# Kernel tuning notes

Measured on AMD Instinct MI355X. Metric: run time of the kernel, lower is better.

## Reference

```python
import jax, jax.numpy as jnp
import numpy as np

B, D, C, T = 2, 1024, 256, 32
H = 8
F = C // H
E = 1024  # time_embed_dim
GROUPS = 32
SCALE = F ** -0.5


def group_norm(x, scale, bias):
    # x: [B, D, C, T]; GroupNorm(32, C) over (channels-in-group, T)
    b, d, c, t = x.shape
    xg = x.reshape(b, d, GROUPS, c // GROUPS, t)
    m = xg.mean(axis=(3, 4), keepdims=True)
    v = xg.var(axis=(3, 4), keepdims=True)
    xn = ((xg - m) * jax.lax.rsqrt(v + 1e-5)).reshape(b, d, c, t)
    return xn * scale[None, None, :, None] + bias[None, None, :, None]


def rpe_R(temb, pairwise, dw, db, tw, tb, ow, ob):
    # pairwise: [B, T, T] int -> R: [B, T, T, H, F]
    pd = pairwise.astype(jnp.float32)
    dist_embs = jnp.stack([
        jnp.log1p(jnp.maximum(pd, 0.0)),
        jnp.log1p(jnp.maximum(-pd, 0.0)),
        (pairwise == 0).astype(jnp.float32),
    ], axis=-1)  # [B, T, T, 3]
    emb = (temb @ tw.T + tb)[:, :, None, :] + (dist_embs @ dw.T + db)  # [B,T,T,C]
    r = jax.nn.silu(emb) @ ow.T + ob
    return r.reshape(r.shape[0], r.shape[1], r.shape[2], H, F)


def setup_inputs() -> dict:
    key = jax.random.key(0)
    ks = jax.random.split(key, 20)
    s = 0.02
    inp = {
        "x": jax.random.normal(ks[0], (B, D, C, T), jnp.float32),
        "temb": jax.random.normal(ks[1], (B, T, E), jnp.float32),
        "norm_scale": jnp.ones((C,), jnp.float32),
        "norm_bias": jnp.zeros((C,), jnp.float32),
        "qkv_w": jax.random.normal(ks[2], (3 * C, C), jnp.float32) * s,
        "qkv_b": jnp.zeros((3 * C,), jnp.float32),
        "proj_w": jax.random.normal(ks[3], (C, C), jnp.float32) * s,
        "proj_b": jnp.zeros((C,), jnp.float32),
        # stacked RPE params for (q, k, v) nets
        "rpe_dist_w": jax.random.normal(ks[4], (3, C, 3), jnp.float32) * s,
        "rpe_dist_b": jnp.zeros((3, C), jnp.float32),
        "rpe_time_w": jax.random.normal(ks[5], (3, C, E), jnp.float32) * s,
        "rpe_time_b": jnp.zeros((3, C), jnp.float32),
        "rpe_out_w": jax.random.normal(ks[6], (3, C, C), jnp.float32) * s,
        "rpe_out_b": jax.random.normal(ks[7], (3, C), jnp.float32) * s,
        "frame_indices": jnp.sort(jax.random.randint(ks[8], (B, T), 0, 100), axis=-1),
    }
    return inp


def reference(x, temb, norm_scale, norm_bias, qkv_w, qkv_b, proj_w, proj_b,
              rpe_dist_w, rpe_dist_b, rpe_time_w, rpe_time_b, rpe_out_w, rpe_out_b,
              frame_indices):
    xn = group_norm(x, norm_scale, norm_bias)          # [B,D,C,T]
    xt = jnp.einsum('BDCT->BDTC', xn)                  # [B,D,T,C]
    qkv = (xt @ qkv_w.T + qkv_b).reshape(B, D, T, 3, H, F)
    qkv = jnp.einsum('BDTtHF->tBDHTF', qkv)
    q, k, v = qkv[0] * SCALE, qkv[1], qkv[2]           # [B,D,H,T,F]

    attn = jnp.einsum('bdhtf,bdhsf->bdhts', q, k)

    pairwise = frame_indices[:, :, None] - frame_indices[:, None, :]  # [B,T,T]
    R_q = rpe_R(temb, pairwise, rpe_dist_w[0], rpe_dist_b[0], rpe_time_w[0], rpe_time_b[0], rpe_out_w[0], rpe_out_b[0])
    R_k = rpe_R(temb, pairwise, rpe_dist_w[1], rpe_dist_b[1], rpe_time_w[1], rpe_time_b[1], rpe_out_w[1], rpe_out_b[1])
    R_v = rpe_R(temb, pairwise, rpe_dist_w[2], rpe_dist_b[2], rpe_time_w[2], rpe_time_b[2], rpe_out_w[2], rpe_out_b[2])

    attn = attn + jnp.einsum('bdhtf,btshf->bdhts', q, R_k)
    # rpe_q: forward_qk on (k*scale) then transpose last two dims
    attn = attn + jnp.einsum('bdhtf,btshf->bdhts', k * SCALE, R_q).swapaxes(-1, -2)

    attn = jax.nn.softmax(attn.astype(jnp.float32), axis=-1).astype(attn.dtype)

    out = jnp.einsum('bdhts,bdhsf->bdhtf', attn, v)
    out = out + jnp.einsum('bdhts,btshf->bdhtf', attn, R_v)

    out = jnp.einsum('BDHTF->BDTHF', out).reshape(B, D, T, C)
    out = out @ proj_w.T + proj_b
    y = xt + out                                       # residual on post-norm x (as in source)
    return jnp.einsum('BDTC->BDCT', y)
```

## Files before the change

### kernel.cpp

```cpp
#include <hip/hip_runtime.h>

#define BB 2
#define DD 1024
#define CC 256
#define TT 32
#define HH 8
#define FF 32
#define EE 1024
#define SCALE 0.17677669529663687f

typedef unsigned short u16;
typedef unsigned int u32;
typedef __attribute__((ext_vector_type(8))) short s8v;
typedef __attribute__((ext_vector_type(4))) float f32x4;

static __device__ __forceinline__ float u2f(u16 u) {
  return __uint_as_float(((u32)u) << 16);
}
static __device__ __forceinline__ u16 f2u(float f) {
  u32 x = __float_as_uint(f);
  x += 0x7fffu + ((x >> 16) & 1u);
  return (u16)(x >> 16);
}
static __device__ __forceinline__ float dot2bf(u32 a, u32 b, float c) {
  float d;
  asm("v_dot2_f32_bf16 %0, %1, %2, %3" : "=v"(d) : "v"(a), "v"(b), "v"(c));
  return d;
}
#define D2(acc, a, b) acc = dot2bf(a, b, acc)

static __device__ __forceinline__ float logits_r(
    const u16* kr,
    uint4 r0, uint4 r1, uint4 r2, uint4 r3,
    uint4 r4, uint4 r5, uint4 r6, uint4 r7,
    uint4 q0, uint4 q1, uint4 q2, uint4 q3) {
  uint4 k0 = *(const uint4*)(kr + 0);
  uint4 k1 = *(const uint4*)(kr + 8);
  uint4 k2 = *(const uint4*)(kr + 16);
  uint4 k3 = *(const uint4*)(kr + 24);
  float xq = 0.f, xr = 0.f, xk = 0.f;
  D2(xq, q0.x, k0.x); D2(xq, q0.y, k0.y); D2(xq, q0.z, k0.z); D2(xq, q0.w, k0.w);
  D2(xq, q1.x, k1.x); D2(xq, q1.y, k1.y); D2(xq, q1.z, k1.z); D2(xq, q1.w, k1.w);
  D2(xq, q2.x, k2.x); D2(xq, q2.y, k2.y); D2(xq, q2.z, k2.z); D2(xq, q2.w, k2.w);
  D2(xq, q3.x, k3.x); D2(xq, q3.y, k3.y); D2(xq, q3.z, k3.z); D2(xq, q3.w, k3.w);
  D2(xr, q0.x, r0.x); D2(xr, q0.y, r0.y); D2(xr, q0.z, r0.z); D2(xr, q0.w, r0.w);
  D2(xr, q1.x, r1.x); D2(xr, q1.y, r1.y); D2(xr, q1.z, r1.z); D2(xr, q1.w, r1.w);
  D2(xr, q2.x, r2.x); D2(xr, q2.y, r2.y); D2(xr, q2.z, r2.z); D2(xr, q2.w, r2.w);
  D2(xr, q3.x, r3.x); D2(xr, q3.y, r3.y); D2(xr, q3.z, r3.z); D2(xr, q3.w, r3.w);
  D2(xk, k0.x, r4.x); D2(xk, k0.y, r4.y); D2(xk, k0.z, r4.z); D2(xk, k0.w, r4.w);
  D2(xk, k1.x, r5.x); D2(xk, k1.y, r5.y); D2(xk, k1.z, r5.z); D2(xk, k1.w, r5.w);
  D2(xk, k2.x, r6.x); D2(xk, k2.y, r6.y); D2(xk, k2.z, r6.z); D2(xk, k2.w, r6.w);
  D2(xk, k3.x, r7.x); D2(xk, k3.y, r7.y); D2(xk, k3.z, r7.z); D2(xk, k3.w, r7.w);
  return xq + xr + xk;
}

static __device__ __forceinline__ float pv_r(
    uint4 p0, uint4 p1, uint4 p2, uint4 p3,
    const u16* vr, uint4 r0, uint4 r1, uint4 r2, uint4 r3) {
  uint4 v0 = *(const uint4*)(vr + 0),  v1 = *(const uint4*)(vr + 8);
  uint4 v2 = *(const uint4*)(vr + 16), v3 = *(const uint4*)(vr + 24);
  float o = 0.f;
  D2(o, p0.x, v0.x); D2(o, p0.y, v0.y); D2(o, p0.z, v0.z); D2(o, p0.w, v0.w);
  D2(o, p1.x, v1.x); D2(o, p1.y, v1.y); D2(o, p1.z, v1.z); D2(o, p1.w, v1.w);
  D2(o, p2.x, v2.x); D2(o, p2.y, v2.y); D2(o, p2.z, v2.z); D2(o, p2.w, v2.w);
  D2(o, p3.x, v3.x); D2(o, p3.y, v3.y); D2(o, p3.z, v3.z); D2(o, p3.w, v3.w);
  D2(o, p0.x, r0.x); D2(o, p0.y, r0.y); D2(o, p0.z, r0.z); D2(o, p0.w, r0.w);
  D2(o, p1.x, r1.x); D2(o, p1.y, r1.y); D2(o, p1.z, r1.z); D2(o, p1.w, r1.w);
  D2(o, p2.x, r2.x); D2(o, p2.y, r2.y); D2(o, p2.z, r2.z); D2(o, p2.w, r2.w);
  D2(o, p3.x, r3.x); D2(o, p3.y, r3.y); D2(o, p3.z, r3.z); D2(o, p3.w, r3.w);
  return o;
}

#define LOADROW8(P, v0, v1, v2, v3, v4, v5, v6, v7)                      \
  v0 = *(const uint4*)((P) + 0);  v1 = *(const uint4*)((P) + 8);         \
  v2 = *(const uint4*)((P) + 16); v3 = *(const uint4*)((P) + 24);        \
  v4 = *(const uint4*)((P) + 32); v5 = *(const uint4*)((P) + 40);        \
  v6 = *(const uint4*)((P) + 48); v7 = *(const uint4*)((P) + 56);
#define LOADROW4(P, v0, v1, v2, v3)                                      \
  v0 = *(const uint4*)((P) + 0);  v1 = *(const uint4*)((P) + 8);         \
  v2 = *(const uint4*)((P) + 16); v3 = *(const uint4*)((P) + 24);

__global__ void k_prep(const float* __restrict__ qw, const float* __restrict__ pw,
                       const float* __restrict__ ow, const float* __restrict__ tw,
                       u16* __restrict__ wpk2, u16* __restrict__ ppk,
                       u16* __restrict__ opk, float* __restrict__ twT) {
  int id = blockIdx.x * 256 + threadIdx.x;
  if (id < 24576) {
    int lane = id & 63, ks = (id >> 6) & 7, tile = id >> 9;
    int hh = tile / 6, r = tile % 6, sec = r >> 1, nt = r & 1;
    int nrow = sec * 256 + hh * 32 + nt * 16 + (lane & 15);
    int k = ks * 32 + (lane >> 4) * 8;
    const float* src = qw + (size_t)nrow * 256 + k;
    u16* dst = wpk2 + (size_t)id * 8;
#pragma unroll
    for (int e = 0; e < 8; ++e) dst[e] = f2u(src[e]);
  } else if (id < 32768) {
    int j = id - 24576;
    int lane = j & 63, ks = (j >> 6) & 7, nt = j >> 9;
    int row = nt * 16 + (lane & 15);
    int k = ks * 32 + (lane >> 4) * 8;
    const float* src = pw + (size_t)row * 256 + k;
    u16* dst = ppk + (size_t)j * 8;
#pragma unroll
    for (int e = 0; e < 8; ++e) dst[e] = f2u(src[e]);
  } else if (id < 57344) {
    int j = id - 32768;
    int lane = j & 63, ks = (j >> 6) & 7, g = j >> 9;
    int n = g >> 4, ntg = g & 15;
    int row = ntg * 16 + (lane & 15);
    int k = ks * 32 + (lane >> 4) * 8;
    const float* src = ow + ((size_t)n * 256 + row) * 256 + k;
    u16* dst = opk + (size_t)j * 8;
#pragma unroll
    for (int e = 0; e < 8; ++e) dst[e] = f2u(src[e]);
  } else {
    int j = id - 57344;
    int n = j >> 16, r = j & 65535;
    int e = r >> 6, c0 = (r & 63) * 4;
    float4 v;
    v.x = tw[((size_t)n * 256 + c0 + 0) * 1024 + e];
    v.y = tw[((size_t)n * 256 + c0 + 1) * 1024 + e];
    v.z = tw[((size_t)n * 256 + c0 + 2) * 1024 + e];
    v.w = tw[((size_t)n * 256 + c0 + 3) * 1024 + e];
    *(float4*)(twT + (size_t)n * 262144 + (size_t)e * 256 + c0) = v;
  }
}

__global__ __launch_bounds__(256) void k_tpe(
    const float* __restrict__ temb, const float* __restrict__ twT,
    const float* __restrict__ tb, const float* __restrict__ dw,
    const float* __restrict__ db, const int* __restrict__ fidx,
    u16* __restrict__ E) {
  int bid = blockIdx.x;
  int t = bid & 31, b = (bid >> 5) & 1, n = bid >> 6;
  __shared__ float st[EE];
  __shared__ int sfi[TT];
  for (int e = threadIdx.x; e < EE; e += 256)
    st[e] = temb[((size_t)b * TT + t) * EE + e];
  if (threadIdx.x < TT) sfi[threadIdx.x] = fidx[b * TT + threadIdx.x];
  __syncthreads();
  int c = threadIdx.x;
  const float* wp = twT + (size_t)n * 262144 + c;
  float a0 = 0.f, a1 = 0.f, a2 = 0.f, a3 = 0.f;
  for (int e = 0; e < EE; e += 4) {
    a0 += st[e + 0] * wp[(size_t)(e + 0) * 256];
    a1 += st[e + 1] * wp[(size_t)(e + 1) * 256];
    a2 += st[e + 2] * wp[(size_t)(e + 2) * 256];
    a3 += st[e + 3] * wp[(size_t)(e + 3) * 256];
  }
  float base = a0 + a1 + a2 + a3 + tb[n * 256 + c] + db[n * 256 + c];
  float dw0 = dw[(n * 256 + c) * 3 + 0];
  float dw1 = dw[(n * 256 + c) * 3 + 1];
  float dw2 = dw[(n * 256 + c) * 3 + 2];
  int ft = sfi[t];
  u16* erow = E + ((size_t)n * 2048 + b * 1024 + t * 32) * 256 + c;
  for (int s = 0; s < TT; ++s) {
    int pd = ft - sfi[s];
    float d0 = log1pf((float)(pd > 0 ? pd : 0));
    float d1 = log1pf((float)(pd < 0 ? -pd : 0));
    float d2 = (pd == 0) ? 1.f : 0.f;
    float e = base + d0 * dw0 + d1 * dw1 + d2 * dw2;
    float se = e / (1.f + expf(-e));
    erow[(size_t)s * 256] = f2u(se);
  }
}

__global__ __launch_bounds__(256) void k_rgemm(
    const u16* __restrict__ E, const u16* __restrict__ opk,
    const float* __restrict__ ob,
    u16* __restrict__ RKQ, u16* __restrict__ Rv) {
  int bid = blockIdx.x;
  int n = bid >> 6, rem = bid & 63;
  int mblk = rem >> 1, nblk = rem & 1;
  int tid = threadIdx.x;
  int w = tid >> 6, lane = tid & 63;
  int l15 = lane & 15, l4 = lane >> 4;
  size_t rowbase = (size_t)n * 2048 + mblk * 64;

  f32x4 acc[2][4];
#pragma unroll
  for (int i = 0; i < 2; ++i) {
    int ntg = nblk * 8 + w * 2 + i;
    float ov = ob[n * 256 + ntg * 16 + l15];
#pragma unroll
    for (int mt = 0; mt < 4; ++mt) acc[i][mt] = (f32x4){ov, ov, ov, ov};
  }
  for (int ks = 0; ks < 8; ++ks) {
    s8v a[4];
#pragma unroll
    for (int mt = 0; mt < 4; ++mt)
      a[mt] = *(const s8v*)(E + (rowbase + mt * 16 + l15) * 256 + ks * 32 + l4 * 8);
#pragma unroll
    for (int i = 0; i < 2; ++i) {
      int ntg = nblk * 8 + w * 2 + i;
      s8v bf = *(const s8v*)(opk + (((size_t)(n * 16 + ntg) * 8 + ks) * 64 + lane) * 8);
#pragma unroll
      for (int mt = 0; mt < 4; ++mt)
        acc[i][mt] = __builtin_amdgcn_mfma_f32_16x16x32_bf16(a[mt], bf, acc[i][mt], 0, 0, 0);
    }
  }
#pragma unroll
  for (int i = 0; i < 2; ++i) {
    int cc = (nblk * 8 + w * 2 + i) * 16 + l15;
    int hh = cc >> 5, f = cc & 31;
#pragma unroll
    for (int mt = 0; mt < 4; ++mt)
#pragma unroll
      for (int r = 0; r < 4; ++r) {
        int rloc = mblk * 64 + mt * 16 + l4 * 4 + r;
        int bb2 = rloc >> 10, tt = (rloc >> 5) & 31, ss = rloc & 31;
        size_t bh = (size_t)(bb2 * 8 + hh);
        float v = acc[i][mt][r];
        if (n == 0)      RKQ[(bh * 1024 + ss * 32 + tt) * 64 + 32 + f] = f2u(v * SCALE);
        else if (n == 1) RKQ[(bh * 1024 + tt * 32 + ss) * 64 + f] = f2u(v);
        else             Rv[((bh * 32 + tt) * 32 + f) * 32 + ss] = f2u(v);
      }
  }
}

__global__ __launch_bounds__(256, 4) void k_gn(
    const float* __restrict__ x, const float* __restrict__ nsc,
    const float* __restrict__ nbi, u16* __restrict__ pun) {
  int bid = blockIdx.x;
  int xcd = bid & 7, jj = bid >> 3;
  int b = xcd >> 2;
  int d = (xcd & 3) * 256 + jj;
  const int tid = threadIdx.x;
  __shared__ u16 xt[TT][264];
  const size_t xbase = ((size_t)(b * DD + d)) * 8192;
  u16* xnp = pun + xbase * 2 + 8192;
  {
    const int c0 = tid >> 3, tq = tid & 7;
    for (int c = c0; c < CC; c += 32) {
      float4 v = *(const float4*)(x + xbase + (size_t)c * TT + tq * 4);
      xt[tq * 4 + 0][c] = f2u(v.x);
      xt[tq * 4 + 1][c] = f2u(v.y);
      xt[tq * 4 + 2][c] = f2u(v.z);
      xt[tq * 4 + 3][c] = f2u(v.w);
    }
  }
  __syncthreads();
  {
    const int c = tid;
    float s = 0.f, s2 = 0.f;
    for (int t = 0; t < TT; ++t) { float v = u2f(xt[t][c]); s += v; s2 += v * v; }
    s += __shfl_xor(s, 1); s2 += __shfl_xor(s2, 1);
    s += __shfl_xor(s, 2); s2 += __shfl_xor(s2, 2);
    s += __shfl_xor(s, 4); s2 += __shfl_xor(s2, 4);
    const float mean = s * (1.f / 256.f);
    const float var = s2 * (1.f / 256.f) - mean * mean;
    const float rs = rsqrtf(var + 1e-5f);
    const float scv = nsc[c] * rs;
    const float biv = nbi[c] - mean * scv;
    for (int t = 0; t < TT; ++t) xt[t][c] = f2u(u2f(xt[t][c]) * scv + biv);
  }
  __syncthreads();
#pragma unroll
  for (int it = 0; it < 4; ++it) {
    int u = it * 256 + tid;
    int t = u >> 5, c = (u & 31) * 8;
    *(uint4*)(xnp + (size_t)u * 8) = *(const uint4*)&xt[t][c];
  }
}

__global__ __launch_bounds__(256, 3) void k_attn(
    u16* __restrict__ pun, const u16* __restrict__ wpk2,
    const float* __restrict__ qkb,
    const u16* __restrict__ RKQ, const u16* __restrict__ Rv) {
  int bid = blockIdx.x;
  int xcd = bid & 7, i5 = bid >> 3;
  int b = xcd >> 2;
  int h = i5 & 7;
  int dg = (xcd & 3) * 64 + (i5 >> 3);
  int d0 = dg * 4;
  const int tid = threadIdx.x;
  __shared__ u16 xsbuf[32 * 264];
  __shared__ u16 qs[4][32][40];
  __shared__ u16 ks_[4][32][40];
  __shared__ u16 vT[4][32][40];
#define XS_(r, c)   xsbuf[(r) * 264 + (c)]
#define ATSP(d, t)  (xsbuf + ((d) * 32 + (t)) * 40)

  const int w = tid >> 6, lane = tid & 63;
  const int l15 = lane & 15, l4 = lane >> 4;
  const int t = tid >> 3, j = tid & 7;
  const size_t bh = (size_t)(b * 8 + h);
  const u16* rp0 = RKQ + (bh * 1024 + (size_t)t * 32 + j) * 64;
  const u16* rv0 = Rv + ((bh * 32 + (size_t)t) * 32 + j) * 32;

  u16* slot0 = pun + ((size_t)(b * DD + d0)) * 16384;

  const u16* xp0 = slot0 + 8192;
  uint4 xr0 = *(const uint4*)(xp0 + (size_t)tid * 8);
  uint4 xr1 = *(const uint4*)(xp0 + (size_t)(256 + tid) * 8);
  uint4 xr2 = *(const uint4*)(xp0 + (size_t)(512 + tid) * 8);
  uint4 xr3 = *(const uint4*)(xp0 + (size_t)(768 + tid) * 8);

  for (int d = 0; d < 4; ++d) {
    *(uint4*)&XS_((tid >> 5), (tid & 31) * 8) = xr0;
    *(uint4*)&XS_(8 + (tid >> 5), (tid & 31) * 8) = xr1;
    *(uint4*)&XS_(16 + (tid >> 5), (tid & 31) * 8) = xr2;
    *(uint4*)&XS_(24 + (tid >> 5), (tid & 31) * 8) = xr3;
    __syncthreads();
    if (d < 3) {
      const u16* nx = slot0 + (size_t)(d + 1) * 16384 + 8192;
      xr0 = *(const uint4*)(nx + (size_t)tid * 8);
      xr1 = *(const uint4*)(nx + (size_t)(256 + tid) * 8);
      xr2 = *(const uint4*)(nx + (size_t)(512 + tid) * 8);
      xr3 = *(const uint4*)(nx + (size_t)(768 + tid) * 8);
    }
#pragma unroll
    for (int i = 0; i < 3; ++i) {
      const int u = w * 3 + i;
      const int sec = u >> 2;
      const int nt = (u >> 1) & 1;
      const int mh = u & 1;
      f32x4 acc = {0.f, 0.f, 0.f, 0.f};
      const u16* wb = wpk2 + ((size_t)((h * 6 + sec * 2 + nt) * 8) * 64 + lane) * 8;
      for (int ks = 0; ks < 8; ++ks) {
        s8v a = *(const s8v*)&XS_(mh * 16 + l15, ks * 32 + l4 * 8);
        s8v bf = *(const s8v*)(wb + (size_t)ks * 512);
        acc = __builtin_amdgcn_mfma_f32_16x16x32_bf16(a, bf, acc, 0, 0, 0);
      }
      const int f = nt * 16 + l15;
      const float bias = qkb[sec * 256 + h * 32 + f];
#pragma unroll
      for (int r = 0; r < 4; ++r) {
        const int tt = mh * 16 + l4 * 4 + r;
        const float val = acc[r] + bias;
        if (sec == 0)      qs[d][tt][f] = f2u(val * SCALE);
        else if (sec == 1) ks_[d][tt][f] = f2u(val);
        else               vT[d][f][tt] = f2u(val);
      }
    }
    __syncthreads();
  }

  uint4 q[4][4];
#pragma unroll
  for (int d = 0; d < 4; ++d) {
    q[d][0] = *(const uint4*)&qs[d][t][0];
    q[d][1] = *(const uint4*)&qs[d][t][8];
    q[d][2] = *(const uint4*)&qs[d][t][16];
    q[d][3] = *(const uint4*)&qs[d][t][24];
  }
  float a[4][4];
  uint4 A0, A1, A2, A3, A4, A5, A6, A7;
  uint4 B0, B1, B2, B3, B4, B5, B6, B7;
  LOADROW8(rp0,          A0, A1, A2, A3, A4, A5, A6, A7)
  LOADROW8(rp0 + 8 * 64, B0, B1, B2, B3, B4, B5, B6, B7)
#pragma unroll
  for (int d = 0; d < 4; ++d)
    a[d][0] = logits_r(&ks_[d][j][0], A0, A1, A2, A3, A4, A5, A6, A7,
                       q[d][0], q[d][1], q[d][2], q[d][3]);
  LOADROW8(rp0 + 16 * 64, A0, A1, A2, A3, A4, A5, A6, A7)
#pragma unroll
  for (int d = 0; d < 4; ++d)
    a[d][1] = logits_r(&ks_[d][j + 8][0], B0, B1, B2, B3, B4, B5, B6, B7,
                       q[d][0], q[d][1], q[d][2], q[d][3]);
  LOADROW8(rp0 + 24 * 64, B0, B1, B2, B3, B4, B5, B6, B7)
#pragma unroll
  for (int d = 0; d < 4; ++d)
    a[d][2] = logits_r(&ks_[d][j + 16][0], A0, A1, A2, A3, A4, A5, A6, A7,
                       q[d][0], q[d][1], q[d][2], q[d][3]);
#pragma unroll
  for (int d = 0; d < 4; ++d)
    a[d][3] = logits_r(&ks_[d][j + 24][0], B0, B1, B2, B3, B4, B5, B6, B7,
                       q[d][0], q[d][1], q[d][2], q[d][3]);

#pragma unroll
  for (int d = 0; d < 4; ++d) {
    float mx = fmaxf(fmaxf(a[d][0], a[d][1]), fmaxf(a[d][2], a[d][3]));
    mx = fmaxf(mx, __shfl_xor(mx, 1));
    mx = fmaxf(mx, __shfl_xor(mx, 2));
    mx = fmaxf(mx, __shfl_xor(mx, 4));
    float e0 = __expf(a[d][0] - mx), e1 = __expf(a[d][1] - mx);
    float e2 = __expf(a[d][2] - mx), e3 = __expf(a[d][3] - mx);
    float sum = e0 + e1 + e2 + e3;
    sum += __shfl_xor(sum, 1);
    sum += __shfl_xor(sum, 2);
    sum += __shfl_xor(sum, 4);
    const float inv = 1.f / sum;
    u16* ap = ATSP(d, t);
    ap[j]      = f2u(e0 * inv);
    ap[j + 8]  = f2u(e1 * inv);
    ap[j + 16] = f2u(e2 * inv);
    ap[j + 24] = f2u(e3 * inv);
  }

  uint4 p[4][4];
#pragma unroll
  for (int d = 0; d < 4; ++d) {
    const u16* ap = ATSP(d, t);
    p[d][0] = *(const uint4*)(ap + 0);
    p[d][1] = *(const uint4*)(ap + 8);
    p[d][2] = *(const uint4*)(ap + 16);
    p[d][3] = *(const uint4*)(ap + 24);
  }
  float o[4][4];
  uint4 VA0, VA1, VA2, VA3, VB0, VB1, VB2, VB3;
  LOADROW4(rv0,          VA0, VA1, VA2, VA3)
  LOADROW4(rv0 + 8 * 32, VB0, VB1, VB2, VB3)
#pragma unroll
  for (int d = 0; d < 4; ++d)
    o[d][0] = pv_r(p[d][0], p[d][1], p[d][2], p[d][3], &vT[d][j][0],
                   VA0, VA1, VA2, VA3);
  LOADROW4(rv0 + 16 * 32, VA0, VA1, VA2, VA3)
#pragma unroll
  for (int d = 0; d < 4; ++d)
    o[d][1] = pv_r(p[d][0], p[d][1], p[d][2], p[d][3], &vT[d][j + 8][0],
                   VB0, VB1, VB2, VB3);
  LOADROW4(rv0 + 24 * 32, VB0, VB1, VB2, VB3)
#pragma unroll
  for (int d = 0; d < 4; ++d)
    o[d][2] = pv_r(p[d][0], p[d][1], p[d][2], p[d][3], &vT[d][j + 16][0],
                   VA0, VA1, VA2, VA3);
#pragma unroll
  for (int d = 0; d < 4; ++d)
    o[d][3] = pv_r(p[d][0], p[d][1], p[d][2], p[d][3], &vT[d][j + 24][0],
                   VB0, VB1, VB2, VB3);

#pragma unroll
  for (int d = 0; d < 4; ++d) {
    u16* op = slot0 + (size_t)d * 16384 + (size_t)t * 256 + h * 32 + j;
    op[0]  = f2u(o[d][0]);
    op[8]  = f2u(o[d][1]);
    op[16] = f2u(o[d][2]);
    op[24] = f2u(o[d][3]);
  }
#undef XS_
#undef ATSP
}

__global__ __launch_bounds__(256, 4) void k_proj(
    u16* __restrict__ pun, const u16* __restrict__ ppk,
    const float* __restrict__ pb, float* __restrict__ out) {
  int bid = blockIdx.x;
  int xcd = bid & 7, jj = bid >> 3;
  int b = xcd >> 2;
  int d = (xcd & 3) * 256 + jj;
  const int tid = threadIdx.x;
  __shared__ u16 obuf[32][264];
  __shared__ u16 xs[32][264];
  const size_t nbase = ((size_t)(b * DD + d)) * 8192;
  u16* slot = pun + nbase * 2;
#pragma unroll
  for (int it = 0; it < 4; ++it) {
    int u = it * 256 + tid;
    int t = u >> 5, c = (u & 31) * 8;
    *(uint4*)&obuf[t][c] = *(const uint4*)(slot + (size_t)u * 8);
    *(uint4*)&xs[t][c]   = *(const uint4*)(slot + 8192 + (size_t)u * 8);
  }
  __syncthreads();

  const int w = tid >> 6, lane = tid & 63;
  const int l15 = lane & 15, l4 = lane >> 4;
  f32x4 pacc[4][2];
#pragma unroll
  for (int i = 0; i < 4; ++i) {
    pacc[i][0] = (f32x4){0.f, 0.f, 0.f, 0.f};
    pacc[i][1] = (f32x4){0.f, 0.f, 0.f, 0.f};
  }
  for (int ks = 0; ks < 8; ++ks) {
    s8v a0 = *(const s8v*)&obuf[l15][ks * 32 + l4 * 8];
    s8v a1 = *(const s8v*)&obuf[16 + l15][ks * 32 + l4 * 8];
#pragma unroll
    for (int i = 0; i < 4; ++i) {
      s8v bf = *(const s8v*)(ppk + ((size_t)((w * 4 + i) * 8 + ks) * 64 + lane) * 8);
      pacc[i][0] = __builtin_amdgcn_mfma_f32_16x16x32_bf16(a0, bf, pacc[i][0], 0, 0, 0);
      pacc[i][1] = __builtin_amdgcn_mfma_f32_16x16x32_bf16(a1, bf, pacc[i][1], 0, 0, 0);
    }
  }
#pragma unroll
  for (int i = 0; i < 4; ++i) {
    const int co = (w * 4 + i) * 16 + l15;
    const float pbv = pb[co];
#pragma unroll
    for (int mt = 0; mt < 2; ++mt) {
      const int t0 = mt * 16 + l4 * 4;
      float4 sv;
      sv.x = pacc[i][mt][0] + u2f(xs[t0 + 0][co]) + pbv;
      sv.y = pacc[i][mt][1] + u2f(xs[t0 + 1][co]) + pbv;
      sv.z = pacc[i][mt][2] + u2f(xs[t0 + 2][co]) + pbv;
      sv.w = pacc[i][mt][3] + u2f(xs[t0 + 3][co]) + pbv;
      *(float4*)(out + nbase + (size_t)co * TT + t0) = sv;
    }
  }
}

extern "C" void kernel_launch(void* const* d_in, const int* in_sizes, int n_in,
                              void* d_out, int out_size, void* d_ws, size_t ws_size,
                              hipStream_t stream) {
  const float* x      = (const float*)d_in[0];
  const float* temb   = (const float*)d_in[1];
  const float* nsc    = (const float*)d_in[2];
  const float* nbi    = (const float*)d_in[3];
  const float* qkv_w  = (const float*)d_in[4];
  const float* qkv_b  = (const float*)d_in[5];
  const float* proj_w = (const float*)d_in[6];
  const float* proj_b = (const float*)d_in[7];
  const float* dw     = (const float*)d_in[8];
  const float* db     = (const float*)d_in[9];
  const float* tw     = (const float*)d_in[10];
  const float* tb     = (const float*)d_in[11];
  const float* ow     = (const float*)d_in[12];
  const float* ob     = (const float*)d_in[13];
  const int*   fidx   = (const int*)d_in[14];
  float* out = (float*)d_out;
  u16* pun = (u16*)d_out;

  float* twT = (float*)d_ws;
  u16* wpk2 = (u16*)(twT + 786432);
  u16* ppk  = wpk2 + 196608;
  u16* opk  = ppk + 65536;
  u16* E    = opk + 196608;
  u16* RKQ  = E + 1572864;
  u16* Rv   = RKQ + 1048576;

  k_prep<<<992, 256, 0, stream>>>(qkv_w, proj_w, ow, tw, wpk2, ppk, opk, twT);
  k_tpe<<<192, 256, 0, stream>>>(temb, twT, tb, dw, db, fidx, E);
  k_rgemm<<<192, 256, 0, stream>>>(E, opk, ob, RKQ, Rv);
  k_gn<<<2048, 256, 0, stream>>>(x, nsc, nbi, pun);
  k_attn<<<4096, 256, 0, stream>>>(pun, wpk2, qkv_b, RKQ, Rv);
  k_proj<<<2048, 256, 0, stream>>>(pun, ppk, proj_b, out);
}
```

Measured before the change: 249.0 us.

## Merge groupnorm, weight packing and time-embedding into one launch; hoist QKV weights

Combines the groupnorm, weight-packing and time-embedding projection kernels into a single heterogeneous launch, chosen by block index, so the independent stages run concurrently and two launches are saved. The time-embedding projection now reads the original row-major weights with coalesced float4 loads and a warp-shuffle reduction, which removes the separate transpose pass and the twT workspace. In the attention kernel the packed QKV weight fragments are loaded into registers once rather than once per d iteration. This raises register pressure in k_attn and may lower occupancy, and the fused kernel carries the larger combined shared-memory footprint in every block.

```diff
diff --git a/kernel.cpp b/kernel.cpp
--- a/kernel.cpp
+++ b/kernel.cpp
@@ -80,88 +80,132 @@
   v0 = *(const uint4*)((P) + 0);  v1 = *(const uint4*)((P) + 8);         \
   v2 = *(const uint4*)((P) + 16); v3 = *(const uint4*)((P) + 24);
 
-__global__ void k_prep(const float* __restrict__ qw, const float* __restrict__ pw,
-                       const float* __restrict__ ow, const float* __restrict__ tw,
-                       u16* __restrict__ wpk2, u16* __restrict__ ppk,
-                       u16* __restrict__ opk, float* __restrict__ twT) {
-  int id = blockIdx.x * 256 + threadIdx.x;
-  if (id < 24576) {
-    int lane = id & 63, ks = (id >> 6) & 7, tile = id >> 9;
-    int hh = tile / 6, r = tile % 6, sec = r >> 1, nt = r & 1;
-    int nrow = sec * 256 + hh * 32 + nt * 16 + (lane & 15);
-    int k = ks * 32 + (lane >> 4) * 8;
-    const float* src = qw + (size_t)nrow * 256 + k;
-    u16* dst = wpk2 + (size_t)id * 8;
-#pragma unroll
-    for (int e = 0; e < 8; ++e) dst[e] = f2u(src[e]);
-  } else if (id < 32768) {
-    int j = id - 24576;
-    int lane = j & 63, ks = (j >> 6) & 7, nt = j >> 9;
-    int row = nt * 16 + (lane & 15);
-    int k = ks * 32 + (lane >> 4) * 8;
-    const float* src = pw + (size_t)row * 256 + k;
-    u16* dst = ppk + (size_t)j * 8;
-#pragma unroll
-    for (int e = 0; e < 8; ++e) dst[e] = f2u(src[e]);
-  } else if (id < 57344) {
-    int j = id - 32768;
-    int lane = j & 63, ks = (j >> 6) & 7, g = j >> 9;
-    int n = g >> 4, ntg = g & 15;
-    int row = ntg * 16 + (lane & 15);
-    int k = ks * 32 + (lane >> 4) * 8;
-    const float* src = ow + ((size_t)n * 256 + row) * 256 + k;
-    u16* dst = opk + (size_t)j * 8;
-#pragma unroll
-    for (int e = 0; e < 8; ++e) dst[e] = f2u(src[e]);
+__global__ __launch_bounds__(256, 4) void k_f0(
+    const float* __restrict__ x, const float* __restrict__ nsc,
+    const float* __restrict__ nbi, u16* __restrict__ pun,
+    const float* __restrict__ qw, const float* __restrict__ pw,
+    const float* __restrict__ ow, const float* __restrict__ tw,
+    const float* __restrict__ temb, const float* __restrict__ tb,
+    const float* __restrict__ dw, const float* __restrict__ db,
+    const int* __restrict__ fidx,
+    u16* __restrict__ wpk2, u16* __restrict__ ppk, u16* __restrict__ opk,
+    u16* __restrict__ E) {
+  const int bid = blockIdx.x;
+  const int tid = threadIdx.x;
+  __shared__ u16 xt[TT][264];
+  __shared__ float st[EE];
+  __shared__ float base_s[CC];
+  __shared__ int sfi[TT];
+
+  if (bid < 2048) {
+    int xcd = bid & 7, jj = bid >> 3;
+    int b = xcd >> 2;
+    int d = (xcd & 3) * 256 + jj;
+    const size_t xbase = ((size_t)(b * DD + d)) * 8192;
+    u16* xnp = pun + xbase * 2 + 8192;
+    {
+      const int c0 = tid >> 3, tq = tid & 7;
+      for (int c = c0; c < CC; c += 32) {
+        float4 v = *(const float4*)(x + xbase + (size_t)c * TT + tq * 4);
+        xt[tq * 4 + 0][c] = f2u(v.x);
+        xt[tq * 4 + 1][c] = f2u(v.y);
+        xt[tq * 4 + 2][c] = f2u(v.z);
+        xt[tq * 4 + 3][c] = f2u(v.w);
+      }
+    }
+    __syncthreads();
+    {
+      const int c = tid;
+      float s = 0.f, s2 = 0.f;
+      for (int t = 0; t < TT; ++t) { float v = u2f(xt[t][c]); s += v; s2 += v * v; }
+      s += __shfl_xor(s, 1); s2 += __shfl_xor(s2, 1);
+      s += __shfl_xor(s, 2); s2 += __shfl_xor(s2, 2);
+      s += __shfl_xor(s, 4); s2 += __shfl_xor(s2, 4);
+      const float mean = s * (1.f / 256.f);
+      const float var = s2 * (1.f / 256.f) - mean * mean;
+      const float rs = rsqrtf(var + 1e-5f);
+      const float scv = nsc[c] * rs;
+      const float biv = nbi[c] - mean * scv;
+      for (int t = 0; t < TT; ++t) xt[t][c] = f2u(u2f(xt[t][c]) * scv + biv);
+    }
+    __syncthreads();
+#pragma unroll
+    for (int it = 0; it < 4; ++it) {
+      int u = it * 256 + tid;
+      int t = u >> 5, c = (u & 31) * 8;
+      *(uint4*)(xnp + (size_t)u * 8) = *(const uint4*)&xt[t][c];
+    }
+  } else if (bid < 2272) {
+    int id = (bid - 2048) * 256 + tid;
+    if (id < 24576) {
+      int lane = id & 63, ks = (id >> 6) & 7, tile = id >> 9;
+      int hh = tile / 6, r = tile % 6, sec = r >> 1, nt = r & 1;
+      int nrow = sec * 256 + hh * 32 + nt * 16 + (lane & 15);
+      int k = ks * 32 + (lane >> 4) * 8;
+      const float* src = qw + (size_t)nrow * 256 + k;
+      u16* dst = wpk2 + (size_t)id * 8;
+#pragma unroll
+      for (int e = 0; e < 8; ++e) dst[e] = f2u(src[e]);
+    } else if (id < 32768) {
+      int j = id - 24576;
+      int lane = j & 63, ks = (j >> 6) & 7, nt = j >> 9;
+      int row = nt * 16 + (lane & 15);
+      int k = ks * 32 + (lane >> 4) * 8;
+      const float* src = pw + (size_t)row * 256 + k;
+      u16* dst = ppk + (size_t)j * 8;
+#pragma unroll
+      for (int e = 0; e < 8; ++e) dst[e] = f2u(src[e]);
+    } else {
+      int j = id - 32768;
+      int lane = j & 63, ks = (j >> 6) & 7, g = j >> 9;
+      int n = g >> 4, ntg = g & 15;
+      int row = ntg * 16 + (lane & 15);
+      int k = ks * 32 + (lane >> 4) * 8;
+      const float* src = ow + ((size_t)n * 256 + row) * 256 + k;
+      u16* dst = opk + (size_t)j * 8;
+#pragma unroll
+      for (int e = 0; e < 8; ++e) dst[e] = f2u(src[e]);
+    }
   } else {
-    int j = id - 57344;
-    int n = j >> 16, r = j & 65535;
-    int e = r >> 6, c0 = (r & 63) * 4;
-    float4 v;
-    v.x = tw[((size_t)n * 256 + c0 + 0) * 1024 + e];
-    v.y = tw[((size_t)n * 256 + c0 + 1) * 1024 + e];
-    v.z = tw[((size_t)n * 256 + c0 + 2) * 1024 + e];
-    v.w = tw[((size_t)n * 256 + c0 + 3) * 1024 + e];
-    *(float4*)(twT + (size_t)n * 262144 + (size_t)e * 256 + c0) = v;
-  }
-}
-
-__global__ __launch_bounds__(256) void k_tpe(
-    const float* __restrict__ temb, const float* __restrict__ twT,
-    const float* __restrict__ tb, const float* __restrict__ dw,
-    const float* __restrict__ db, const int* __restrict__ fidx,
-    u16* __restrict__ E) {
-  int bid = blockIdx.x;
-  int t = bid & 31, b = (bid >> 5) & 1, n = bid >> 6;
-  __shared__ float st[EE];
-  __shared__ int sfi[TT];
-  for (int e = threadIdx.x; e < EE; e += 256)
-    st[e] = temb[((size_t)b * TT + t) * EE + e];
-  if (threadIdx.x < TT) sfi[threadIdx.x] = fidx[b * TT + threadIdx.x];
-  __syncthreads();
-  int c = threadIdx.x;
-  const float* wp = twT + (size_t)n * 262144 + c;
-  float a0 = 0.f, a1 = 0.f, a2 = 0.f, a3 = 0.f;
-  for (int e = 0; e < EE; e += 4) {
-    a0 += st[e + 0] * wp[(size_t)(e + 0) * 256];
-    a1 += st[e + 1] * wp[(size_t)(e + 1) * 256];
-    a2 += st[e + 2] * wp[(size_t)(e + 2) * 256];
-    a3 += st[e + 3] * wp[(size_t)(e + 3) * 256];
-  }
-  float base = a0 + a1 + a2 + a3 + tb[n * 256 + c] + db[n * 256 + c];
-  float dw0 = dw[(n * 256 + c) * 3 + 0];
-  float dw1 = dw[(n * 256 + c) * 3 + 1];
-  float dw2 = dw[(n * 256 + c) * 3 + 2];
-  int ft = sfi[t];
-  u16* erow = E + ((size_t)n * 2048 + b * 1024 + t * 32) * 256 + c;
-  for (int s = 0; s < TT; ++s) {
-    int pd = ft - sfi[s];
-    float d0 = log1pf((float)(pd > 0 ? pd : 0));
-    float d1 = log1pf((float)(pd < 0 ? -pd : 0));
-    float d2 = (pd == 0) ? 1.f : 0.f;
-    float e = base + d0 * dw0 + d1 * dw1 + d2 * dw2;
-    float se = e / (1.f + expf(-e));
-    erow[(size_t)s * 256] = f2u(se);
+    int bid3 = bid - 2272;
+    int t = bid3 & 31, b = (bid3 >> 5) & 1, n = bid3 >> 6;
+    for (int e = tid; e < EE; e += 256)
+      st[e] = temb[((size_t)b * TT + t) * EE + e];
+    if (tid < TT) sfi[tid] = fidx[b * TT + tid];
+    __syncthreads();
+    const int g = tid & 7, cl = tid >> 3;
+#pragma unroll
+    for (int pass = 0; pass < 8; ++pass) {
+      const int c = pass * 32 + cl;
+      const float* wr = tw + ((size_t)n * 256 + c) * 1024 + g * 4;
+      float acc = 0.f;
+      for (int step = 0; step < 32; ++step) {
+        float4 wv = *(const float4*)(wr + step * 32);
+        float4 sv = *(const float4*)(st + g * 4 + step * 32);
+        acc += sv.x * wv.x + sv.y * wv.y + sv.z * wv.z + sv.w * wv.w;
+      }
+      acc += __shfl_xor(acc, 1);
+      acc += __shfl_xor(acc, 2);
+      acc += __shfl_xor(acc, 4);
+      if (g == 0) base_s[c] = acc;
+    }
+    __syncthreads();
+    const int c = tid;
+    float base = base_s[c] + tb[n * 256 + c] + db[n * 256 + c];
+    float dw0 = dw[(n * 256 + c) * 3 + 0];
+    float dw1 = dw[(n * 256 + c) * 3 + 1];
+    float dw2 = dw[(n * 256 + c) * 3 + 2];
+    int ft = sfi[t];
+    u16* erow = E + ((size_t)n * 2048 + b * 1024 + t * 32) * 256 + c;
+    for (int s = 0; s < TT; ++s) {
+      int pd = ft - sfi[s];
+      float d0 = log1pf((float)(pd > 0 ? pd : 0));
+      float d1 = log1pf((float)(pd < 0 ? -pd : 0));
+      float d2 = (pd == 0) ? 1.f : 0.f;
+      float e = base + d0 * dw0 + d1 * dw1 + d2 * dw2;
+      float se = e / (1.f + expf(-e));
+      erow[(size_t)s * 256] = f2u(se);
+    }
   }
 }
 
@@ -215,51 +259,6 @@
         else if (n == 1) RKQ[(bh * 1024 + tt * 32 + ss) * 64 + f] = f2u(v);
         else             Rv[((bh * 32 + tt) * 32 + f) * 32 + ss] = f2u(v);
       }
-  }
-}
-
-__global__ __launch_bounds__(256, 4) void k_gn(
-    const float* __restrict__ x, const float* __restrict__ nsc,
-    const float* __restrict__ nbi, u16* __restrict__ pun) {
-  int bid = blockIdx.x;
-  int xcd = bid & 7, jj = bid >> 3;
-  int b = xcd >> 2;
-  int d = (xcd & 3) * 256 + jj;
-  const int tid = threadIdx.x;
-  __shared__ u16 xt[TT][264];
-  const size_t xbase = ((size_t)(b * DD + d)) * 8192;
-  u16* xnp = pun + xbase * 2 + 8192;
-  {
-    const int c0 = tid >> 3, tq = tid & 7;
-    for (int c = c0; c < CC; c += 32) {
-      float4 v = *(const float4*)(x + xbase + (size_t)c * TT + tq * 4);
-      xt[tq * 4 + 0][c] = f2u(v.x);
-      xt[tq * 4 + 1][c] = f2u(v.y);
-      xt[tq * 4 + 2][c] = f2u(v.z);
-      xt[tq * 4 + 3][c] = f2u(v.w);
-    }
-  }
-  __syncthreads();
-  {
-    const int c = tid;
-    float s = 0.f, s2 = 0.f;
-    for (int t = 0; t < TT; ++t) { float v = u2f(xt[t][c]); s += v; s2 += v * v; }
-    s += __shfl_xor(s, 1); s2 += __shfl_xor(s2, 1);
-    s += __shfl_xor(s, 2); s2 += __shfl_xor(s2, 2);
-    s += __shfl_xor(s, 4); s2 += __shfl_xor(s2, 4);
-    const float mean = s * (1.f / 256.f);
-    const float var = s2 * (1.f / 256.f) - mean * mean;
-    const float rs = rsqrtf(var + 1e-5f);
-    const float scv = nsc[c] * rs;
-    const float biv = nbi[c] - mean * scv;
-    for (int t = 0; t < TT; ++t) xt[t][c] = f2u(u2f(xt[t][c]) * scv + biv);
-  }
-  __syncthreads();
-#pragma unroll
-  for (int it = 0; it < 4; ++it) {
-    int u = it * 256 + tid;
-    int t = u >> 5, c = (u & 31) * 8;
-    *(uint4*)(xnp + (size_t)u * 8) = *(const uint4*)&xt[t][c];
   }
 }
 
@@ -296,6 +295,17 @@
   uint4 xr2 = *(const uint4*)(xp0 + (size_t)(512 + tid) * 8);
   uint4 xr3 = *(const uint4*)(xp0 + (size_t)(768 + tid) * 8);
 
+  s8v wf[3][8];
+#pragma unroll
+  for (int i = 0; i < 3; ++i) {
+    const int u = w * 3 + i;
+    const int sec = u >> 2, nt = (u >> 1) & 1;
+    const u16* wb = wpk2 + ((size_t)((h * 6 + sec * 2 + nt) * 8) * 64 + lane) * 8;
+#pragma unroll
+    for (int ks = 0; ks < 8; ++ks)
+      wf[i][ks] = *(const s8v*)(wb + (size_t)ks * 512);
+  }
+
   for (int d = 0; d < 4; ++d) {
     *(uint4*)&XS_((tid >> 5), (tid & 31) * 8) = xr0;
     *(uint4*)&XS_(8 + (tid >> 5), (tid & 31) * 8) = xr1;
@@ -316,11 +326,10 @@
       const int nt = (u >> 1) & 1;
       const int mh = u & 1;
       f32x4 acc = {0.f, 0.f, 0.f, 0.f};
-      const u16* wb = wpk2 + ((size_t)((h * 6 + sec * 2 + nt) * 8) * 64 + lane) * 8;
+#pragma unroll
       for (int ks = 0; ks < 8; ++ks) {
         s8v a = *(const s8v*)&XS_(mh * 16 + l15, ks * 32 + l4 * 8);
-        s8v bf = *(const s8v*)(wb + (size_t)ks * 512);
-        acc = __builtin_amdgcn_mfma_f32_16x16x32_bf16(a, bf, acc, 0, 0, 0);
+        acc = __builtin_amdgcn_mfma_f32_16x16x32_bf16(a, wf[i][ks], acc, 0, 0, 0);
       }
       const int f = nt * 16 + l15;
       const float bias = qkb[sec * 256 + h * 32 + f];
@@ -509,18 +518,16 @@
   float* out = (float*)d_out;
   u16* pun = (u16*)d_out;
 
-  float* twT = (float*)d_ws;
-  u16* wpk2 = (u16*)(twT + 786432);
+  u16* wpk2 = (u16*)d_ws;
   u16* ppk  = wpk2 + 196608;
   u16* opk  = ppk + 65536;
   u16* E    = opk + 196608;
   u16* RKQ  = E + 1572864;
   u16* Rv   = RKQ + 1048576;
 
-  k_prep<<<992, 256, 0, stream>>>(qkv_w, proj_w, ow, tw, wpk2, ppk, opk, twT);
-  k_tpe<<<192, 256, 0, stream>>>(temb, twT, tb, dw, db, fidx, E);
+  k_f0<<<2464, 256, 0, stream>>>(x, nsc, nbi, pun, qkv_w, proj_w, ow, tw,
+                                 temb, tb, dw, db, fidx, wpk2, ppk, opk, E);
   k_rgemm<<<192, 256, 0, stream>>>(E, opk, ob, RKQ, Rv);
-  k_gn<<<2048, 256, 0, stream>>>(x, nsc, nbi, pun);
   k_attn<<<4096, 256, 0, stream>>>(pun, wpk2, qkv_b, RKQ, Rv);
   k_proj<<<2048, 256, 0, stream>>>(pun, ppk, proj_b, out);
 }
```

Result: faster. 236.4 us (-5.0%).
